# Performance work log

Hardware: AMD Instinct MI355X
Metric: run time of the kernel (lower is better)

Reference implementation:

```python
import jax, jax.numpy as jnp
import numpy as np

K = 8192
D = 256


def setup_inputs() -> dict:
    key = jax.random.key(0)
    k1, k2 = jax.random.split(key)
    z_e_x = jax.random.normal(k1, (32, 32, 32, D), dtype=jnp.float32)
    # matches torch init: uniform(-1/K, 1/K)
    codebook = jax.random.uniform(k2, (K, D), dtype=jnp.float32,
                                  minval=-1.0 / K, maxval=1.0 / K)
    return {"z_e_x": z_e_x, "codebook": codebook}


def reference(z_e_x, codebook):
    # vq(): nearest-neighbor codebook indices under squared L2 distance.
    flat = z_e_x.reshape(-1, z_e_x.shape[-1])            # [N, D]
    # ||z - e||^2 = ||z||^2 - 2 z.e + ||e||^2 ; ||z||^2 constant over argmin
    dots = flat @ codebook.T                              # [N, K]
    cb_sq = jnp.sum(codebook * codebook, axis=-1)         # [K]
    dist = cb_sq[None, :] - 2.0 * dots                    # [N, K]
    indices = jnp.argmin(dist, axis=-1)                   # [N] int
    return indices.reshape(z_e_x.shape[:-1])              # latent index grid
```

## Files before the change

### kernel.cpp

```cpp
#include <hip/hip_runtime.h>
#include <hip/hip_fp16.h>


#define N_Q   32768
#define K_CB  8192
#define D_DIM 256

typedef _Float16 half8 __attribute__((ext_vector_type(8)));
typedef float    f32x4 __attribute__((ext_vector_type(4)));

__device__ __forceinline__ void gl_lds16(const _Float16* g, _Float16* l) {
  __builtin_amdgcn_global_load_lds(
      (const __attribute__((address_space(1))) unsigned int*)g,
      (__attribute__((address_space(3))) unsigned int*)l, 16, 0, 0);
}


__global__ void vq_prep_z(const float* __restrict__ z, _Float16* __restrict__ zpk) {
  int t = blockIdx.x * 256 + threadIdx.x;
  int l = t & 63, g = t >> 6;
  int qb = g >> 6, q16 = (g >> 3) & 7, kk = g & 7;
  int row = qb * 128 + q16 * 16 + (l & 15);
  int kc  = kk * 32 + (l >> 4) * 8;
  const float4* zp = (const float4*)(z + (size_t)row * 256 + kc);
  float4 a = zp[0], b = zp[1];
  float xs[8] = {a.x, a.y, a.z, a.w, b.x, b.y, b.z, b.w};
  half8 hh, ll;
#pragma unroll
  for (int j = 0; j < 8; ++j) {
    float x = xs[j] * 16.0f;
    _Float16 hj = (_Float16)x;
    hh[j] = hj; ll[j] = (_Float16)(x - (float)hj);
  }
  ((half8*)zpk)[(size_t)g * 128 + l]      = hh;
  ((half8*)zpk)[(size_t)g * 128 + 64 + l] = ll;
}

__global__ void vq_prep_e(const float* __restrict__ cb, _Float16* __restrict__ epk) {
  int t = blockIdx.x * 256 + threadIdx.x;
  int l = t & 63, g = t >> 6;
  int c16 = g >> 3, kk = g & 7;
  int code = c16 * 16 + (l & 15);
  int kc   = kk * 32 + (l >> 4) * 8;
  const float4* ep = (const float4*)(cb + (size_t)code * 256 + kc);
  float4 a = ep[0], b = ep[1];
  float xs[8] = {a.x, a.y, a.z, a.w, b.x, b.y, b.z, b.w};
  half8 hh, ll;
#pragma unroll
  for (int j = 0; j < 8; ++j) {
    float x = xs[j] * 32768.0f;
    _Float16 hj = (_Float16)x;
    hh[j] = hj; ll[j] = (_Float16)(x - (float)hj);
  }
  ((half8*)epk)[(size_t)g * 128 + l]      = hh;
  ((half8*)epk)[(size_t)g * 128 + 64 + l] = ll;
}

__global__ void vq_prep_cbs(const float* __restrict__ cb, float* __restrict__ cbs) {
  int w = threadIdx.x >> 6, lane = threadIdx.x & 63;
  int code = blockIdx.x * 4 + w;
  float4 v = ((const float4*)cb)[code * 64 + lane];
  float ss = v.x * v.x + v.y * v.y + v.z * v.z + v.w * v.w;
#pragma unroll
  for (int off = 1; off < 64; off <<= 1) ss += __shfl_xor(ss, off);
  if (lane == 0) cbs[code] = ss * 524288.0f;
}

__global__ __launch_bounds__(512, 2)
void vq_main(const _Float16* __restrict__ zpk, const _Float16* __restrict__ epk,
             const float* __restrict__ cbs, int* __restrict__ out) {
  __shared__ __align__(16) char smem[131072];
  _Float16* const A = (_Float16*)smem;

  const int tid  = threadIdx.x;
  const int lane = tid & 63;
  const int w    = tid >> 6;
  const int h    = w >> 2;
  const int v    = w & 1;
  const int p    = (w >> 1) & 1;
  const int q    = lane & 15;
  const int quad = lane >> 4;
  const int qb   = blockIdx.x;
  const int q0   = qb * 128;

  {
    const _Float16* src = zpk + (size_t)qb * 65536;
    for (int c = 0; c < 16; ++c) {
      const int off = (c * 512 + tid) * 8;
      gl_lds16(src + off, A + off);
    }
  }
  __syncthreads();

  const half8* const Ab = (const half8*)A + h * 4096 + lane;
  const half8* const eb = (const half8*)epk + (size_t)p * 262144
                        + (size_t)v * 4096 + lane;

  float    rd[16];
  unsigned rc[16];
#pragma unroll
  for (int i = 0; i < 16; ++i) { rd[i] = 3.0e38f; rc[i] = 0u; }

  for (int i = 0; i < 32; ++i) {
    const int ct   = p * 32 + i;
    const int col0 = ct * 128 + v * 64 + q;
    const half8* const ebi = eb + (size_t)i * 8192;

    float cbsv[4];
#pragma unroll
    for (int nt = 0; nt < 4; ++nt) cbsv[nt] = cbs[col0 + nt * 16];

    f32x4 acc[4][4];
#pragma unroll
    for (int mt = 0; mt < 4; ++mt)
#pragma unroll
      for (int nt = 0; nt < 4; ++nt)
        acc[mt][nt] = (f32x4){0.f, 0.f, 0.f, 0.f};

#pragma unroll 2
    for (int kk = 0; kk < 8; ++kk) {
      half8 bh[4], bl[4], ah[4], al[4];
#pragma unroll
      for (int nt = 0; nt < 4; ++nt) {
        bh[nt] = ebi[nt * 1024 + kk * 128];
        bl[nt] = ebi[nt * 1024 + kk * 128 + 64];
      }
#pragma unroll
      for (int mt = 0; mt < 4; ++mt) {
        ah[mt] = Ab[mt * 1024 + kk * 128];
        al[mt] = Ab[mt * 1024 + kk * 128 + 64];
      }
#pragma unroll
      for (int mt = 0; mt < 4; ++mt)
#pragma unroll
        for (int nt = 0; nt < 4; ++nt) {
          acc[mt][nt] = __builtin_amdgcn_mfma_f32_16x16x32_f16(ah[mt], bh[nt], acc[mt][nt], 0, 0, 0);
          acc[mt][nt] = __builtin_amdgcn_mfma_f32_16x16x32_f16(ah[mt], bl[nt], acc[mt][nt], 0, 0, 0);
          acc[mt][nt] = __builtin_amdgcn_mfma_f32_16x16x32_f16(al[mt], bh[nt], acc[mt][nt], 0, 0, 0);
        }
    }

#pragma unroll
    for (int mt = 0; mt < 4; ++mt)
#pragma unroll
      for (int r = 0; r < 4; ++r) {
        float d = fmaf(-2.0f, acc[mt][0][r], cbsv[0]);
        unsigned cidx = (unsigned)col0;
#pragma unroll
        for (int nt = 1; nt < 4; ++nt) {
          float dn = fmaf(-2.0f, acc[mt][nt][r], cbsv[nt]);
          if (dn < d) { d = dn; cidx = (unsigned)(col0 + nt * 16); }
        }
        int ri = mt * 4 + r;
        if (d < rd[ri]) { rd[ri] = d; rc[ri] = cidx; }
      }
  }

  __syncthreads();
  float*    const redD = (float*)smem;
  unsigned* const redC = (unsigned*)(smem + 2048);

#pragma unroll
  for (int ri = 0; ri < 16; ++ri) {
    float d = rd[ri]; unsigned cidx = rc[ri];
#pragma unroll
    for (int off = 1; off < 16; off <<= 1) {
      float od = __shfl_xor(d, off);
      unsigned oc = __shfl_xor(cidx, off);
      if (od < d || (od == d && oc < cidx)) { d = od; cidx = oc; }
    }
    if (q == 0) {
      int row = h * 64 + (ri >> 2) * 16 + quad * 4 + (ri & 3);
      redD[(w & 3) * 128 + row] = d;
      redC[(w & 3) * 128 + row] = cidx;
    }
  }
  __syncthreads();
  if (tid < 128) {
    float d0 = redD[tid]; unsigned c0 = redC[tid];
#pragma unroll
    for (int s = 1; s < 4; ++s) {
      float ds = redD[s * 128 + tid]; unsigned cs = redC[s * 128 + tid];
      if (ds < d0 || (ds == d0 && cs < c0)) { d0 = ds; c0 = cs; }
    }
    out[q0 + tid] = (int)c0;
  }
}

extern "C" void kernel_launch(void* const* d_in, const int* in_sizes, int n_in,
                              void* d_out, int out_size, void* d_ws, size_t ws_size,
                              hipStream_t stream) {
  const float* z  = (const float*)d_in[0];
  const float* cb = (const float*)d_in[1];
  char* ws = (char*)d_ws;
  _Float16* zpk = (_Float16*)(ws);
  _Float16* epk = (_Float16*)(ws + (size_t)32 * 1024 * 1024);
  float*    cbs = (float*)(ws + (size_t)40 * 1024 * 1024);

  hipLaunchKernelGGL(vq_prep_z,   dim3(4096), dim3(256), 0, stream, z, zpk);
  hipLaunchKernelGGL(vq_prep_e,   dim3(1024), dim3(256), 0, stream, cb, epk);
  hipLaunchKernelGGL(vq_prep_cbs, dim3(2048), dim3(256), 0, stream, cb, cbs);
  hipLaunchKernelGGL(vq_main,     dim3(256),  dim3(512), 0, stream,
                     zpk, epk, cbs, (int*)d_out);
}
```

Before: 400.9 us.

## Switch matmul tiles from 16x16x32 to 32x32x16 MFMA with repacked operands

Replaces the 16x16x32 f16 MFMA tiling with 32x32x16 instructions, using a 2x2 grid of 32x32 accumulator tiles per wave instead of 4x4 of 16x16. Both prep kernels repack the split-f16 operands into the 32-row, 16-wide-k layout the new instruction expects, and the argmin epilogue and cross-lane reduction are remapped to the 32x32 output layout. The aim is fewer MFMA issues and operand fetches per flop. In exchange each lane tracks 32 running minima instead of 16 and the reduction needs one more shuffle step, which raises register pressure. The code-tile base index also changes from i to ct, which alters how the p half of the waves addresses epk.

```diff
diff --git a/kernel.cpp b/kernel.cpp
--- a/kernel.cpp
+++ b/kernel.cpp
@@ -7,7 +7,7 @@
 #define D_DIM 256
 
 typedef _Float16 half8 __attribute__((ext_vector_type(8)));
-typedef float    f32x4 __attribute__((ext_vector_type(4)));
+typedef float    f32x16 __attribute__((ext_vector_type(16)));
 
 __device__ __forceinline__ void gl_lds16(const _Float16* g, _Float16* l) {
   __builtin_amdgcn_global_load_lds(
@@ -19,9 +19,9 @@
 __global__ void vq_prep_z(const float* __restrict__ z, _Float16* __restrict__ zpk) {
   int t = blockIdx.x * 256 + threadIdx.x;
   int l = t & 63, g = t >> 6;
-  int qb = g >> 6, q16 = (g >> 3) & 7, kk = g & 7;
-  int row = qb * 128 + q16 * 16 + (l & 15);
-  int kc  = kk * 32 + (l >> 4) * 8;
+  int qb = g >> 6, q32 = (g >> 4) & 3, kk = g & 15;
+  int row = qb * 128 + q32 * 32 + (l & 31);
+  int kc  = kk * 16 + (l >> 5) * 8;
   const float4* zp = (const float4*)(z + (size_t)row * 256 + kc);
   float4 a = zp[0], b = zp[1];
   float xs[8] = {a.x, a.y, a.z, a.w, b.x, b.y, b.z, b.w};
@@ -39,9 +39,9 @@
 __global__ void vq_prep_e(const float* __restrict__ cb, _Float16* __restrict__ epk) {
   int t = blockIdx.x * 256 + threadIdx.x;
   int l = t & 63, g = t >> 6;
-  int c16 = g >> 3, kk = g & 7;
-  int code = c16 * 16 + (l & 15);
-  int kc   = kk * 32 + (l >> 4) * 8;
+  int c32 = g >> 4, kk = g & 15;
+  int code = c32 * 32 + (l & 31);
+  int kc   = kk * 16 + (l >> 5) * 8;
   const float4* ep = (const float4*)(cb + (size_t)code * 256 + kc);
   float4 a = ep[0], b = ep[1];
   float xs[8] = {a.x, a.y, a.z, a.w, b.x, b.y, b.z, b.w};
@@ -75,16 +75,16 @@
   const int tid  = threadIdx.x;
   const int lane = tid & 63;
   const int w    = tid >> 6;
-  const int h    = w >> 2;
   const int v    = w & 1;
   const int p    = (w >> 1) & 1;
-  const int q    = lane & 15;
-  const int quad = lane >> 4;
-  const int qb   = blockIdx.x;
-  const int q0   = qb * 128;
+  const int h    = w >> 2;
+  const int c32l = lane & 31;
+  const int hi   = lane >> 5;
+  const int b    = blockIdx.x;
+  const int q0   = b * 128;
 
   {
-    const _Float16* src = zpk + (size_t)qb * 65536;
+    const _Float16* src = zpk + (size_t)b * 65536;
     for (int c = 0; c < 16; ++c) {
       const int off = (c * 512 + tid) * 8;
       gl_lds16(src + off, A + off);
@@ -93,65 +93,61 @@
   __syncthreads();
 
   const half8* const Ab = (const half8*)A + h * 4096 + lane;
-  const half8* const eb = (const half8*)epk + (size_t)p * 262144
-                        + (size_t)v * 4096 + lane;
-
-  float    rd[16];
-  unsigned rc[16];
-#pragma unroll
-  for (int i = 0; i < 16; ++i) { rd[i] = 3.0e38f; rc[i] = 0u; }
+  const half8* const eb = (const half8*)epk + (size_t)v * 4096 + lane;
+
+  float    rd[32];
+  unsigned rc[32];
+#pragma unroll
+  for (int i = 0; i < 32; ++i) { rd[i] = 3.0e38f; rc[i] = 0u; }
 
   for (int i = 0; i < 32; ++i) {
     const int ct   = p * 32 + i;
-    const int col0 = ct * 128 + v * 64 + q;
-    const half8* const ebi = eb + (size_t)i * 8192;
-
-    float cbsv[4];
-#pragma unroll
-    for (int nt = 0; nt < 4; ++nt) cbsv[nt] = cbs[col0 + nt * 16];
-
-    f32x4 acc[4][4];
-#pragma unroll
-    for (int mt = 0; mt < 4; ++mt)
-#pragma unroll
-      for (int nt = 0; nt < 4; ++nt)
-        acc[mt][nt] = (f32x4){0.f, 0.f, 0.f, 0.f};
+    const int col0 = ct * 128 + v * 64 + c32l;
+    const half8* const ebi = eb + (size_t)ct * 8192;
+
+    float cbsv[2];
+#pragma unroll
+    for (int nt = 0; nt < 2; ++nt) cbsv[nt] = cbs[col0 + nt * 32];
+
+    f32x16 acc[2][2];
+#pragma unroll
+    for (int mt = 0; mt < 2; ++mt)
+#pragma unroll
+      for (int nt = 0; nt < 2; ++nt)
+        acc[mt][nt] = (f32x16)(0.0f);
 
 #pragma unroll 2
-    for (int kk = 0; kk < 8; ++kk) {
-      half8 bh[4], bl[4], ah[4], al[4];
-#pragma unroll
-      for (int nt = 0; nt < 4; ++nt) {
-        bh[nt] = ebi[nt * 1024 + kk * 128];
-        bl[nt] = ebi[nt * 1024 + kk * 128 + 64];
+    for (int kk = 0; kk < 16; ++kk) {
+      half8 bh[2], bl[2], ah[2], al[2];
+#pragma unroll
+      for (int nt = 0; nt < 2; ++nt) {
+        bh[nt] = ebi[nt * 2048 + kk * 128];
+        bl[nt] = ebi[nt * 2048 + kk * 128 + 64];
       }
 #pragma unroll
-      for (int mt = 0; mt < 4; ++mt) {
-        ah[mt] = Ab[mt * 1024 + kk * 128];
-        al[mt] = Ab[mt * 1024 + kk * 128 + 64];
+      for (int mt = 0; mt < 2; ++mt) {
+        ah[mt] = Ab[mt * 2048 + kk * 128];
+        al[mt] = Ab[mt * 2048 + kk * 128 + 64];
       }
 #pragma unroll
-      for (int mt = 0; mt < 4; ++mt)
-#pragma unroll
-        for (int nt = 0; nt < 4; ++nt) {
-          acc[mt][nt] = __builtin_amdgcn_mfma_f32_16x16x32_f16(ah[mt], bh[nt], acc[mt][nt], 0, 0, 0);
-          acc[mt][nt] = __builtin_amdgcn_mfma_f32_16x16x32_f16(ah[mt], bl[nt], acc[mt][nt], 0, 0, 0);
-          acc[mt][nt] = __builtin_amdgcn_mfma_f32_16x16x32_f16(al[mt], bh[nt], acc[mt][nt], 0, 0, 0);
+      for (int mt = 0; mt < 2; ++mt)
+#pragma unroll
+        for (int nt = 0; nt < 2; ++nt) {
+          acc[mt][nt] = __builtin_amdgcn_mfma_f32_32x32x16_f16(ah[mt], bh[nt], acc[mt][nt], 0, 0, 0);
+          acc[mt][nt] = __builtin_amdgcn_mfma_f32_32x32x16_f16(ah[mt], bl[nt], acc[mt][nt], 0, 0, 0);
+          acc[mt][nt] = __builtin_amdgcn_mfma_f32_32x32x16_f16(al[mt], bh[nt], acc[mt][nt], 0, 0, 0);
         }
     }
 
 #pragma unroll
-    for (int mt = 0; mt < 4; ++mt)
-#pragma unroll
-      for (int r = 0; r < 4; ++r) {
+    for (int mt = 0; mt < 2; ++mt)
+#pragma unroll
+      for (int r = 0; r < 16; ++r) {
         float d = fmaf(-2.0f, acc[mt][0][r], cbsv[0]);
         unsigned cidx = (unsigned)col0;
-#pragma unroll
-        for (int nt = 1; nt < 4; ++nt) {
-          float dn = fmaf(-2.0f, acc[mt][nt][r], cbsv[nt]);
-          if (dn < d) { d = dn; cidx = (unsigned)(col0 + nt * 16); }
-        }
-        int ri = mt * 4 + r;
+        float dn = fmaf(-2.0f, acc[mt][1][r], cbsv[1]);
+        if (dn < d) { d = dn; cidx = (unsigned)(col0 + 32); }
+        int ri = mt * 16 + r;
         if (d < rd[ri]) { rd[ri] = d; rc[ri] = cidx; }
       }
   }
@@ -161,16 +157,17 @@
   unsigned* const redC = (unsigned*)(smem + 2048);
 
 #pragma unroll
-  for (int ri = 0; ri < 16; ++ri) {
+  for (int ri = 0; ri < 32; ++ri) {
     float d = rd[ri]; unsigned cidx = rc[ri];
 #pragma unroll
-    for (int off = 1; off < 16; off <<= 1) {
+    for (int off = 1; off < 32; off <<= 1) {
       float od = __shfl_xor(d, off);
       unsigned oc = __shfl_xor(cidx, off);
       if (od < d || (od == d && oc < cidx)) { d = od; cidx = oc; }
     }
-    if (q == 0) {
-      int row = h * 64 + (ri >> 2) * 16 + quad * 4 + (ri & 3);
+    if (c32l == 0) {
+      int mt = ri >> 4, r = ri & 15;
+      int row = h * 64 + mt * 32 + (r & 3) + 8 * (r >> 2) + 4 * hi;
       redD[(w & 3) * 128 + row] = d;
       redC[(w & 3) * 128 + row] = cidx;
     }
```

New measurement: 464.6 us. +15.9%, slower.

## Fuse z/codebook/norm prep kernels into one LDS-staged prep kernel

Applied to the files above, without the earlier changes.

Merges the three preprocessing kernels (z split-fp16 packing, codebook packing, codebook squared norms) into a single launch. Each block stages a 16-row tile in LDS with coalesced float4 loads, then emits the hi/lo fp16 packed layout from shared memory. The codebook norms come from the same staged tile, so the codebook is no longer read twice from global memory. The main kernel's codebook indexing is rewritten to match the new packed layout. This trades two launches and strided global reads for extra LDS traffic and a block-level sync.

```diff
diff --git a/kernel.cpp b/kernel.cpp
--- a/kernel.cpp
+++ b/kernel.cpp
@@ -16,54 +16,54 @@
 }
 
 
-__global__ void vq_prep_z(const float* __restrict__ z, _Float16* __restrict__ zpk) {
-  int t = blockIdx.x * 256 + threadIdx.x;
-  int l = t & 63, g = t >> 6;
-  int qb = g >> 6, q16 = (g >> 3) & 7, kk = g & 7;
-  int row = qb * 128 + q16 * 16 + (l & 15);
-  int kc  = kk * 32 + (l >> 4) * 8;
-  const float4* zp = (const float4*)(z + (size_t)row * 256 + kc);
-  float4 a = zp[0], b = zp[1];
-  float xs[8] = {a.x, a.y, a.z, a.w, b.x, b.y, b.z, b.w};
-  half8 hh, ll;
-#pragma unroll
-  for (int j = 0; j < 8; ++j) {
-    float x = xs[j] * 16.0f;
-    _Float16 hj = (_Float16)x;
-    hh[j] = hj; ll[j] = (_Float16)(x - (float)hj);
-  }
-  ((half8*)zpk)[(size_t)g * 128 + l]      = hh;
-  ((half8*)zpk)[(size_t)g * 128 + 64 + l] = ll;
-}
-
-__global__ void vq_prep_e(const float* __restrict__ cb, _Float16* __restrict__ epk) {
-  int t = blockIdx.x * 256 + threadIdx.x;
-  int l = t & 63, g = t >> 6;
-  int c16 = g >> 3, kk = g & 7;
-  int code = c16 * 16 + (l & 15);
-  int kc   = kk * 32 + (l >> 4) * 8;
-  const float4* ep = (const float4*)(cb + (size_t)code * 256 + kc);
-  float4 a = ep[0], b = ep[1];
-  float xs[8] = {a.x, a.y, a.z, a.w, b.x, b.y, b.z, b.w};
-  half8 hh, ll;
-#pragma unroll
-  for (int j = 0; j < 8; ++j) {
-    float x = xs[j] * 32768.0f;
-    _Float16 hj = (_Float16)x;
-    hh[j] = hj; ll[j] = (_Float16)(x - (float)hj);
-  }
-  ((half8*)epk)[(size_t)g * 128 + l]      = hh;
-  ((half8*)epk)[(size_t)g * 128 + 64 + l] = ll;
-}
-
-__global__ void vq_prep_cbs(const float* __restrict__ cb, float* __restrict__ cbs) {
-  int w = threadIdx.x >> 6, lane = threadIdx.x & 63;
-  int code = blockIdx.x * 4 + w;
-  float4 v = ((const float4*)cb)[code * 64 + lane];
-  float ss = v.x * v.x + v.y * v.y + v.z * v.z + v.w * v.w;
-#pragma unroll
-  for (int off = 1; off < 64; off <<= 1) ss += __shfl_xor(ss, off);
-  if (lane == 0) cbs[code] = ss * 524288.0f;
+__global__ __launch_bounds__(256)
+void vq_prep(const float* __restrict__ z, const float* __restrict__ cb,
+             _Float16* __restrict__ zpk, _Float16* __restrict__ epk,
+             float* __restrict__ cbs) {
+  __shared__ float ld[16 * 264];
+  const int  t   = threadIdx.x;
+  const bool isZ = (blockIdx.x < 2048);
+  const int  blk = isZ ? blockIdx.x : (blockIdx.x - 2048);
+  const float* src  = (isZ ? z : cb) + (size_t)blk * 4096;
+  const float scale = isZ ? 16.0f : 32768.0f;
+  _Float16*   dst   = (isZ ? zpk : epk) + (size_t)blk * 8192;
+
+#pragma unroll
+  for (int c = 0; c < 4; ++c) {
+    const int f   = c * 256 + t;
+    const int row = f >> 6, c4 = f & 63;
+    float4 v = ((const float4*)src)[f];
+    *(float4*)&ld[row * 264 + c4 * 4] = v;
+  }
+  __syncthreads();
+
+  if (!isZ) {
+    const int ci = t >> 4, seg = t & 15;
+    float s = 0.f;
+#pragma unroll
+    for (int j = 0; j < 16; ++j) {
+      float x = ld[ci * 264 + seg * 16 + j];
+      s = fmaf(x, x, s);
+    }
+#pragma unroll
+    for (int off = 1; off < 16; off <<= 1) s += __shfl_xor(s, off);
+    if (seg == 0) cbs[blk * 16 + ci] = s * 524288.0f;
+  }
+
+#pragma unroll
+  for (int c = 0; c < 4; ++c) {
+    const int o    = c * 256 + t;
+    const int kk   = o >> 7, r = o & 127, hl = r >> 6, l = r & 63;
+    const int lrow = l & 15, k0 = kk * 32 + (l >> 4) * 8;
+    half8 hv;
+#pragma unroll
+    for (int j = 0; j < 8; ++j) {
+      float x = ld[lrow * 264 + k0 + j] * scale;
+      _Float16 hj = (_Float16)x;
+      hv[j] = hl ? (_Float16)(x - (float)hj) : hj;
+    }
+    ((half8*)dst)[o] = hv;
+  }
 }
 
 __global__ __launch_bounds__(512, 2)
@@ -93,8 +93,7 @@
   __syncthreads();
 
   const half8* const Ab = (const half8*)A + h * 4096 + lane;
-  const half8* const eb = (const half8*)epk + (size_t)p * 262144
-                        + (size_t)v * 4096 + lane;
+  const half8* const eb = (const half8*)epk + (size_t)v * 4096 + lane;
 
   float    rd[16];
   unsigned rc[16];
@@ -104,7 +103,7 @@
   for (int i = 0; i < 32; ++i) {
     const int ct   = p * 32 + i;
     const int col0 = ct * 128 + v * 64 + q;
-    const half8* const ebi = eb + (size_t)i * 8192;
+    const half8* const ebi = eb + (size_t)ct * 8192;
 
     float cbsv[4];
 #pragma unroll
@@ -197,9 +196,8 @@
   _Float16* epk = (_Float16*)(ws + (size_t)32 * 1024 * 1024);
   float*    cbs = (float*)(ws + (size_t)40 * 1024 * 1024);
 
-  hipLaunchKernelGGL(vq_prep_z,   dim3(4096), dim3(256), 0, stream, z, zpk);
-  hipLaunchKernelGGL(vq_prep_e,   dim3(1024), dim3(256), 0, stream, cb, epk);
-  hipLaunchKernelGGL(vq_prep_cbs, dim3(2048), dim3(256), 0, stream, cb, cbs);
-  hipLaunchKernelGGL(vq_main,     dim3(256),  dim3(512), 0, stream,
+  hipLaunchKernelGGL(vq_prep, dim3(2560), dim3(256), 0, stream,
+                     z, cb, zpk, epk, cbs);
+  hipLaunchKernelGGL(vq_main, dim3(256),  dim3(512), 0, stream,
                      zpk, epk, cbs, (int*)d_out);
 }
```

Measured after the change: 393.4 us. About the same (-1.9%).

## Fuse z split-conversion into main kernel and merge codebook prep kernels

Applied to the files above, without the earlier changes.

Drops the separate z pre-pack kernel: the main kernel now reads fp32 z directly, splits it into hi/lo fp16, and writes the packed tile straight into LDS. It also merges the codebook split-conversion and squared-norm kernels into one launch. This removes the 32 MB zpk round trip through global memory and two kernel launches. The cost is that the main kernel's prologue now does the conversion work with ordinary loads instead of async global-to-LDS copies. The epk indexing is also simplified to use the column tile index directly.

```diff
diff --git a/kernel.cpp b/kernel.cpp
--- a/kernel.cpp
+++ b/kernel.cpp
@@ -9,65 +9,51 @@
 typedef _Float16 half8 __attribute__((ext_vector_type(8)));
 typedef float    f32x4 __attribute__((ext_vector_type(4)));
 
-__device__ __forceinline__ void gl_lds16(const _Float16* g, _Float16* l) {
-  __builtin_amdgcn_global_load_lds(
-      (const __attribute__((address_space(1))) unsigned int*)g,
-      (__attribute__((address_space(3))) unsigned int*)l, 16, 0, 0);
+
+__global__ __launch_bounds__(256)
+void vq_prep_e(const float* __restrict__ cb, _Float16* __restrict__ epk,
+               float* __restrict__ cbs) {
+  const int t = threadIdx.x, c16 = blockIdx.x;
+
+#pragma unroll
+  for (int it = 0; it < 2; ++it) {
+    const int s   = it * 256 + t;
+    const int kk  = s >> 6, l = s & 63;
+    const int row = c16 * 16 + (l & 15);
+    const int k0  = kk * 32 + (l >> 4) * 8;
+    const float4* ep = (const float4*)(cb + (size_t)row * 256 + k0);
+    float4 a = ep[0], b = ep[1];
+    float xs[8] = {a.x, a.y, a.z, a.w, b.x, b.y, b.z, b.w};
+    half8 hh, ll;
+#pragma unroll
+    for (int j = 0; j < 8; ++j) {
+      float x = xs[j] * 32768.0f;
+      _Float16 hj = (_Float16)x;
+      hh[j] = hj; ll[j] = (_Float16)(x - (float)hj);
+    }
+    half8* outg = (half8*)epk + (size_t)(c16 * 8 + kk) * 128;
+    outg[l]      = hh;
+    outg[64 + l] = ll;
+  }
+
+  {
+    const int ci = t >> 4, seg = t & 15;
+    const int row = c16 * 16 + ci;
+    const float4* ep = (const float4*)(cb + (size_t)row * 256 + seg * 16);
+    float s = 0.f;
+#pragma unroll
+    for (int u = 0; u < 4; ++u) {
+      float4 v = ep[u];
+      s = fmaf(v.x, v.x, fmaf(v.y, v.y, fmaf(v.z, v.z, fmaf(v.w, v.w, s))));
+    }
+#pragma unroll
+    for (int off = 1; off < 16; off <<= 1) s += __shfl_xor(s, off);
+    if (seg == 0) cbs[row] = s * 524288.0f;
+  }
 }
 
-
-__global__ void vq_prep_z(const float* __restrict__ z, _Float16* __restrict__ zpk) {
-  int t = blockIdx.x * 256 + threadIdx.x;
-  int l = t & 63, g = t >> 6;
-  int qb = g >> 6, q16 = (g >> 3) & 7, kk = g & 7;
-  int row = qb * 128 + q16 * 16 + (l & 15);
-  int kc  = kk * 32 + (l >> 4) * 8;
-  const float4* zp = (const float4*)(z + (size_t)row * 256 + kc);
-  float4 a = zp[0], b = zp[1];
-  float xs[8] = {a.x, a.y, a.z, a.w, b.x, b.y, b.z, b.w};
-  half8 hh, ll;
-#pragma unroll
-  for (int j = 0; j < 8; ++j) {
-    float x = xs[j] * 16.0f;
-    _Float16 hj = (_Float16)x;
-    hh[j] = hj; ll[j] = (_Float16)(x - (float)hj);
-  }
-  ((half8*)zpk)[(size_t)g * 128 + l]      = hh;
-  ((half8*)zpk)[(size_t)g * 128 + 64 + l] = ll;
-}
-
-__global__ void vq_prep_e(const float* __restrict__ cb, _Float16* __restrict__ epk) {
-  int t = blockIdx.x * 256 + threadIdx.x;
-  int l = t & 63, g = t >> 6;
-  int c16 = g >> 3, kk = g & 7;
-  int code = c16 * 16 + (l & 15);
-  int kc   = kk * 32 + (l >> 4) * 8;
-  const float4* ep = (const float4*)(cb + (size_t)code * 256 + kc);
-  float4 a = ep[0], b = ep[1];
-  float xs[8] = {a.x, a.y, a.z, a.w, b.x, b.y, b.z, b.w};
-  half8 hh, ll;
-#pragma unroll
-  for (int j = 0; j < 8; ++j) {
-    float x = xs[j] * 32768.0f;
-    _Float16 hj = (_Float16)x;
-    hh[j] = hj; ll[j] = (_Float16)(x - (float)hj);
-  }
-  ((half8*)epk)[(size_t)g * 128 + l]      = hh;
-  ((half8*)epk)[(size_t)g * 128 + 64 + l] = ll;
-}
-
-__global__ void vq_prep_cbs(const float* __restrict__ cb, float* __restrict__ cbs) {
-  int w = threadIdx.x >> 6, lane = threadIdx.x & 63;
-  int code = blockIdx.x * 4 + w;
-  float4 v = ((const float4*)cb)[code * 64 + lane];
-  float ss = v.x * v.x + v.y * v.y + v.z * v.z + v.w * v.w;
-#pragma unroll
-  for (int off = 1; off < 64; off <<= 1) ss += __shfl_xor(ss, off);
-  if (lane == 0) cbs[code] = ss * 524288.0f;
-}
-
 __global__ __launch_bounds__(512, 2)
-void vq_main(const _Float16* __restrict__ zpk, const _Float16* __restrict__ epk,
+void vq_main(const float* __restrict__ z, const _Float16* __restrict__ epk,
              const float* __restrict__ cbs, int* __restrict__ out) {
   __shared__ __align__(16) char smem[131072];
   _Float16* const A = (_Float16*)smem;
@@ -84,17 +70,32 @@
   const int q0   = qb * 128;
 
   {
-    const _Float16* src = zpk + (size_t)qb * 65536;
-    for (int c = 0; c < 16; ++c) {
-      const int off = (c * 512 + tid) * 8;
-      gl_lds16(src + off, A + off);
+    const float* zsrc = z + (size_t)q0 * 256;
+#pragma unroll
+    for (int it = 0; it < 8; ++it) {
+      const int s   = it * 512 + tid;
+      const int g   = s >> 6, l = s & 63;
+      const int row = (g >> 3) * 16 + (l & 15);
+      const int k0  = (g & 7) * 32 + (l >> 4) * 8;
+      const float4* zp = (const float4*)(zsrc + (size_t)row * 256 + k0);
+      float4 a = zp[0], b = zp[1];
+      float xs[8] = {a.x, a.y, a.z, a.w, b.x, b.y, b.z, b.w};
+      half8 hh, ll;
+#pragma unroll
+      for (int j = 0; j < 8; ++j) {
+        float x = xs[j] * 16.0f;
+        _Float16 hj = (_Float16)x;
+        hh[j] = hj; ll[j] = (_Float16)(x - (float)hj);
+      }
+      half8* const Ag = (half8*)A + g * 128;
+      Ag[l]      = hh;
+      Ag[64 + l] = ll;
     }
   }
   __syncthreads();
 
   const half8* const Ab = (const half8*)A + h * 4096 + lane;
-  const half8* const eb = (const half8*)epk + (size_t)p * 262144
-                        + (size_t)v * 4096 + lane;
+  const half8* const eb = (const half8*)epk + (size_t)v * 4096 + lane;
 
   float    rd[16];
   unsigned rc[16];
@@ -104,7 +105,7 @@
   for (int i = 0; i < 32; ++i) {
     const int ct   = p * 32 + i;
     const int col0 = ct * 128 + v * 64 + q;
-    const half8* const ebi = eb + (size_t)i * 8192;
+    const half8* const ebi = eb + (size_t)ct * 8192;
 
     float cbsv[4];
 #pragma unroll
@@ -193,13 +194,10 @@
   const float* z  = (const float*)d_in[0];
   const float* cb = (const float*)d_in[1];
   char* ws = (char*)d_ws;
-  _Float16* zpk = (_Float16*)(ws);
-  _Float16* epk = (_Float16*)(ws + (size_t)32 * 1024 * 1024);
-  float*    cbs = (float*)(ws + (size_t)40 * 1024 * 1024);
-
-  hipLaunchKernelGGL(vq_prep_z,   dim3(4096), dim3(256), 0, stream, z, zpk);
-  hipLaunchKernelGGL(vq_prep_e,   dim3(1024), dim3(256), 0, stream, cb, epk);
-  hipLaunchKernelGGL(vq_prep_cbs, dim3(2048), dim3(256), 0, stream, cb, cbs);
-  hipLaunchKernelGGL(vq_main,     dim3(256),  dim3(512), 0, stream,
-                     zpk, epk, cbs, (int*)d_out);
+  _Float16* epk = (_Float16*)(ws);
+  float*    cbs = (float*)(ws + (size_t)16 * 1024 * 1024);
+
+  hipLaunchKernelGGL(vq_prep_e, dim3(512), dim3(256), 0, stream, cb, epk, cbs);
+  hipLaunchKernelGGL(vq_main,   dim3(256), dim3(512), 0, stream,
+                     z, epk, cbs, (int*)d_out);
 }
```

After: 385.7 us. 3.8% less time.
